# Kernel optimization log

Hardware: AMD Instinct MI355X
Metric: run time of the kernel (lower is better)

Reference implementation:

```python
import jax, jax.numpy as jnp
import numpy as np


def _to_complex(t):
    # last dim 2 = (real, imag) -> complex64
    return jax.lax.complex(t[..., 0], t[..., 1])


def setup_inputs() -> dict:
    key = jax.random.key(0)
    k1, k2, k3, k4 = jax.random.split(key, 4)
    N, C_out, C_in, H, Wf = 2, 64, 3, 256, 129  # Wf = 256//2 + 1 (rfft width)
    X = jax.random.normal(k1, (N, 1, C_in, H, Wf, 2), dtype=jnp.float32)
    D = jax.random.normal(k2, (N, C_out, C_in, H, Wf, 2), dtype=jnp.float32)
    Y = jax.random.normal(k3, (N, C_out, 1, H, Wf, 2), dtype=jnp.float32)
    # alpha is a positive penalty weight; offset away from 0 to avoid blow-up in Z/alpha
    alpha = jax.random.uniform(k4, (N, 1, 1, 1), dtype=jnp.float32) + 0.5
    x_size = np.array([256, 256], dtype=np.int64)  # spatial size for irfft2
    return {"X": X, "D": D, "Y": Y, "alpha": alpha, "x_size": x_size}


def reference(X, D, Y, alpha, x_size):
    C_in = X.shape[2]
    Xc = _to_complex(X)  # (N,1,C_in,H,Wf)
    Dc = _to_complex(D)  # (N,C_out,C_in,H,Wf)
    Yc = _to_complex(Y)  # (N,C_out,1,H,Wf)
    # alpha.unsqueeze(-1).unsqueeze(-1)/C_in: in complex repr one extra axis suffices
    a = (alpha / C_in)[..., None]  # (N,1,1,1,1), real, broadcasts over (N,C_out,C_in,H,Wf)
    Dconj = jnp.conj(Dc)
    Z = Yc * Dc + a * Xc  # (N,C_out,C_in,H,Wf)
    factor1 = Z / a
    numerator = jnp.sum(Dconj * Z, axis=2, keepdims=True)  # (N,C_out,1,H,Wf)
    # csum adds a real scalar (alpha^2) to the real part only
    denominator = a * jnp.sum(Dconj * Dc, axis=2, keepdims=True) + a ** 2
    factor2 = Dc * (numerator / denominator)  # (N,C_out,C_in,H,Wf)
    Xhat = jnp.mean(factor1 - factor2, axis=1)  # (N,C_in,H,Wf)
    Hs, Ws = int(x_size[0]), int(x_size[1])
    # torch.irfft(signal_ndim=2, normalized=False) == full (1/n-normalized) inverse rfft2
    return jnp.fft.irfftn(Xhat, s=(Hs, Ws), axes=(-2, -1))
```

## Files before the change

kernel.cpp:

```cpp
#include <hip/hip_runtime.h>
#include <math.h>

#define H_   256
#define Wf_  129
#define HWf_ 33024
#define CIN_ 3
#define COUT_ 64
#define TW_  0.0245436926f

typedef float f32x4 __attribute__((ext_vector_type(4)));

__global__ __launch_bounds__(256) void solve_stage1(
    const float* __restrict__ X, const float* __restrict__ D,
    const float* __restrict__ Y, const float* __restrict__ alpha,
    float* __restrict__ Xhat)
{
    const int tid  = threadIdx.x;
    const int pl   = tid & 15;
    const int cog  = tid >> 4;
    const int pair = blockIdx.x * 16 + pl;
    const int pos0 = pair * 2;
    const int n    = pos0 / HWf_;
    const int hw0  = pos0 - n * HWf_;

    const float a    = alpha[n] * (1.0f / 3.0f);
    const float inva = 1.0f / a;
    const float a2   = a * a;

    f32x4 x[3];
#pragma unroll
    for (int ci = 0; ci < 3; ++ci)
        x[ci] = *(const f32x4*)(X + ((size_t)(n * 3 + ci) * HWf_ + hw0) * 2);

    const int co0 = cog * 4;
    const float* Dp = D + ((size_t)(n * 64 + co0) * 3) * (HWf_ * 2) + hw0 * 2;
    const float* Yp = Y + ((size_t)(n * 64 + co0)) * (HWf_ * 2) + hw0 * 2;

    float acc[12];
#pragma unroll
    for (int q = 0; q < 12; ++q) acc[q] = 0.f;

#pragma unroll
    for (int co = 0; co < 4; ++co) {
        f32x4 y  = __builtin_nontemporal_load(
                       (const f32x4*)(Yp + (size_t)co * (HWf_ * 2)));
        f32x4 d0 = __builtin_nontemporal_load(
                       (const f32x4*)(Dp + (size_t)(co * 3 + 0) * (HWf_ * 2)));
        f32x4 d1 = __builtin_nontemporal_load(
                       (const f32x4*)(Dp + (size_t)(co * 3 + 1) * (HWf_ * 2)));
        f32x4 d2 = __builtin_nontemporal_load(
                       (const f32x4*)(Dp + (size_t)(co * 3 + 2) * (HWf_ * 2)));

        {
            float s2 = d0[0]*d0[0] + d0[1]*d0[1] + d1[0]*d1[0] + d1[1]*d1[1]
                     + d2[0]*d2[0] + d2[1]*d2[1];
            float sr = d0[0]*x[0][0] + d0[1]*x[0][1] + d1[0]*x[1][0] + d1[1]*x[1][1]
                     + d2[0]*x[2][0] + d2[1]*x[2][1];
            float si = d0[0]*x[0][1] - d0[1]*x[0][0] + d1[0]*x[1][1] - d1[1]*x[1][0]
                     + d2[0]*x[2][1] - d2[1]*x[2][0];
            float nr = y[0] * s2 + a * sr, ni = y[1] * s2 + a * si;
            float invden = 1.0f / (a * s2 + a2);
            float tr = y[0] * inva - nr * invden;
            float ti = y[1] * inva - ni * invden;
            acc[0] += d0[0]*tr - d0[1]*ti;  acc[1] += d0[0]*ti + d0[1]*tr;
            acc[2] += d1[0]*tr - d1[1]*ti;  acc[3] += d1[0]*ti + d1[1]*tr;
            acc[4] += d2[0]*tr - d2[1]*ti;  acc[5] += d2[0]*ti + d2[1]*tr;
        }
        {
            float s2 = d0[2]*d0[2] + d0[3]*d0[3] + d1[2]*d1[2] + d1[3]*d1[3]
                     + d2[2]*d2[2] + d2[3]*d2[3];
            float sr = d0[2]*x[0][2] + d0[3]*x[0][3] + d1[2]*x[1][2] + d1[3]*x[1][3]
                     + d2[2]*x[2][2] + d2[3]*x[2][3];
            float si = d0[2]*x[0][3] - d0[3]*x[0][2] + d1[2]*x[1][3] - d1[3]*x[1][2]
                     + d2[2]*x[2][3] - d2[3]*x[2][2];
            float nr = y[2] * s2 + a * sr, ni = y[3] * s2 + a * si;
            float invden = 1.0f / (a * s2 + a2);
            float tr = y[2] * inva - nr * invden;
            float ti = y[3] * inva - ni * invden;
            acc[6]  += d0[2]*tr - d0[3]*ti;  acc[7]  += d0[2]*ti + d0[3]*tr;
            acc[8]  += d1[2]*tr - d1[3]*ti;  acc[9]  += d1[2]*ti + d1[3]*tr;
            acc[10] += d2[2]*tr - d2[3]*ti;  acc[11] += d2[2]*ti + d2[3]*tr;
        }
    }

    __shared__ float red[16 * 192];
    {
        const int base = cog * 192 + pl * 12;
#pragma unroll
        for (int q = 0; q < 12; ++q) red[base + q] = acc[q];
    }
    __syncthreads();

    if (tid < 192) {
        float s = 0.f;
#pragma unroll
        for (int c = 0; c < 16; ++c) s += red[c * 192 + tid];
        const int P   = tid / 12;
        const int r   = tid - P * 12;
        const int pos = r / 6;
        const int rr  = r - pos * 6;
        const int ci  = rr >> 1;
        const int cc  = rr & 1;
        const int gp  = (blockIdx.x * 16 + P) * 2 + pos;
        const int hw  = gp - n * HWf_;
        const size_t o = ((size_t)(n * 3 + ci) * HWf_ + hw) * 2 + cc;
        Xhat[o] = X[o] + s * (1.0f / 64.0f);
    }
}

__global__ __launch_bounds__(128) void solve_stage2(
    const float2* __restrict__ in, float2* __restrict__ out)
{
    __shared__ float2 col[256];

    const int b    = blockIdx.x;
    const int n_ci = b / Wf_;
    const int w    = b - n_ci * Wf_;
    const int t    = threadIdx.x;

    const float2* src = in + (size_t)n_ci * HWf_ + w;
    col[t]       = src[t * Wf_];
    col[t + 128] = src[(t + 128) * Wf_];
    __syncthreads();

    float wc, wsn;
    sincosf((float)t * TW_, &wsn, &wc);

    float ar = 0.f, ai = 0.f, br = 0.f, bi = 0.f;
    for (int kb = 0; kb < 8; ++kb) {
        const int k0 = kb * 32;
        float tr, ti;
        {
            const int m = (t * k0) & 255;
            float s, c; sincosf((float)m * TW_, &s, &c);
            tr = c; ti = s;
        }
#pragma unroll
        for (int j = 0; j < 32; ++j) {
            const float2 v = col[k0 + j];
            const float pr = v.x * tr - v.y * ti;
            const float pi = v.x * ti + v.y * tr;
            ar += pr; ai += pi;
            if ((k0 + j) & 1) { br -= pr; bi -= pi; }
            else             { br += pr; bi += pi; }
            const float nt = tr * wc - ti * wsn;
            ti = tr * wsn + ti * wc;
            tr = nt;
        }
    }

    float2* dst = out + (size_t)n_ci * HWf_ + w;
    dst[t * Wf_]         = make_float2(ar * (1.0f / 256.0f), ai * (1.0f / 256.0f));
    dst[(t + 128) * Wf_] = make_float2(br * (1.0f / 256.0f), bi * (1.0f / 256.0f));
}

__global__ __launch_bounds__(128) void solve_stage3(
    const float2* __restrict__ in, float* __restrict__ out)
{
    __shared__ float2 row[Wf_];

    const int b = blockIdx.x;
    const int t = threadIdx.x;

    row[t] = in[(size_t)b * Wf_ + t];
    if (t == 0) row[128] = in[(size_t)b * Wf_ + 128];
    __syncthreads();

    float wc, wsn;
    sincosf((float)t * TW_, &wsn, &wc);

    float sa = 0.f, sb = 0.f;
    for (int kb = 0; kb < 4; ++kb) {
        const int k0 = kb * 32;
        float tr, ti;
        {
            const int m = (t * k0) & 255;
            float s, c; sincosf((float)m * TW_, &s, &c);
            tr = c; ti = s;
        }
#pragma unroll
        for (int j = 0; j < 32; ++j) {
            const float2 v = row[k0 + j];
            const float pr = v.x * tr - v.y * ti;
            sa += pr;
            if ((k0 + j) & 1) sb -= pr; else sb += pr;
            const float nt = tr * wc - ti * wsn;
            ti = tr * wsn + ti * wc;
            tr = nt;
        }
    }

    const float sgn  = (t & 1) ? -1.0f : 1.0f;
    const float base = -0.5f * row[0].x + sgn * 0.5f * row[128].x;
    out[(size_t)b * 256 + t]       = (sa + base) * (1.0f / 128.0f);
    out[(size_t)b * 256 + t + 128] = (sb + base) * (1.0f / 128.0f);
}

extern "C" void kernel_launch(void* const* d_in, const int* in_sizes, int n_in,
                              void* d_out, int out_size, void* d_ws, size_t ws_size,
                              hipStream_t stream) {
    const float* X     = (const float*)d_in[0];
    const float* D     = (const float*)d_in[1];
    const float* Y     = (const float*)d_in[2];
    const float* alpha = (const float*)d_in[3];

    float* ws1 = (float*)d_ws;
    float2* ws2 = (float2*)(ws1 + (size_t)CIN_ * 2 * HWf_ * 2);

    solve_stage1<<<2064, 256, 0, stream>>>(X, D, Y, alpha, ws1);
    solve_stage2<<<2 * CIN_ * Wf_, 128, 0, stream>>>((const float2*)ws1, ws2);
    solve_stage3<<<2 * CIN_ * H_, 128, 0, stream>>>(ws2, (float*)d_out);
}
```

Measured before the change: 204.4 us.

## Store intermediate spectrum column-major so column FFT reads contiguously

Stage 1 now writes Xhat transposed to (n,ci,w,h), so the column inverse DFT in stage 2 reads and writes contiguous 256-element columns instead of reads strided by Wf. Stage 2 packs two columns per 256-thread block. Stage 3 now does the strided gather from the transposed layout when loading each row, and writes its output with nontemporal stores. The aim is cheaper memory access in the DFT stages, at the cost of scattered writes in stage 1 and strided reads in stage 3.

```diff
diff --git a/kernel.cpp b/kernel.cpp
--- a/kernel.cpp
+++ b/kernel.cpp
@@ -103,24 +103,26 @@
         const int cc  = rr & 1;
         const int gp  = (blockIdx.x * 16 + P) * 2 + pos;
         const int hw  = gp - n * HWf_;
-        const size_t o = ((size_t)(n * 3 + ci) * HWf_ + hw) * 2 + cc;
-        Xhat[o] = X[o] + s * (1.0f / 64.0f);
-    }
-}
-
-__global__ __launch_bounds__(128) void solve_stage2(
+        const int h   = hw / Wf_;
+        const int w   = hw - h * Wf_;
+        const size_t so = ((size_t)(n * 3 + ci) * HWf_ + hw) * 2 + cc;
+        const size_t o = (((size_t)(n * 3 + ci) * Wf_ + w) * H_ + h) * 2 + cc;
+        Xhat[o] = X[so] + s * (1.0f / 64.0f);
+    }
+}
+
+__global__ __launch_bounds__(256) void solve_stage2(
     const float2* __restrict__ in, float2* __restrict__ out)
 {
-    __shared__ float2 col[256];
-
-    const int b    = blockIdx.x;
-    const int n_ci = b / Wf_;
-    const int w    = b - n_ci * Wf_;
-    const int t    = threadIdx.x;
-
-    const float2* src = in + (size_t)n_ci * HWf_ + w;
-    col[t]       = src[t * Wf_];
-    col[t + 128] = src[(t + 128) * Wf_];
+    __shared__ float2 col[2][256];
+
+    const int b   = blockIdx.x;
+    const int sub = threadIdx.x >> 7;
+    const int t   = threadIdx.x & 127;
+
+    const float2* src = in + ((size_t)b * 2 + sub) * H_;
+    col[sub][t]       = src[t];
+    col[sub][t + 128] = src[t + 128];
     __syncthreads();
 
     float wc, wsn;
@@ -137,7 +139,7 @@
         }
 #pragma unroll
         for (int j = 0; j < 32; ++j) {
-            const float2 v = col[k0 + j];
+            const float2 v = col[sub][k0 + j];
             const float pr = v.x * tr - v.y * ti;
             const float pi = v.x * ti + v.y * tr;
             ar += pr; ai += pi;
@@ -149,9 +151,9 @@
         }
     }
 
-    float2* dst = out + (size_t)n_ci * HWf_ + w;
-    dst[t * Wf_]         = make_float2(ar * (1.0f / 256.0f), ai * (1.0f / 256.0f));
-    dst[(t + 128) * Wf_] = make_float2(br * (1.0f / 256.0f), bi * (1.0f / 256.0f));
+    float2* dst = out + ((size_t)b * 2 + sub) * H_;
+    dst[t]       = make_float2(ar * (1.0f / 256.0f), ai * (1.0f / 256.0f));
+    dst[t + 128] = make_float2(br * (1.0f / 256.0f), bi * (1.0f / 256.0f));
 }
 
 __global__ __launch_bounds__(128) void solve_stage3(
@@ -159,11 +161,13 @@
 {
     __shared__ float2 row[Wf_];
 
-    const int b = blockIdx.x;
-    const int t = threadIdx.x;
-
-    row[t] = in[(size_t)b * Wf_ + t];
-    if (t == 0) row[128] = in[(size_t)b * Wf_ + 128];
+    const int b    = blockIdx.x;
+    const int n_ci = b >> 8;
+    const int h    = b & 255;
+    const int t    = threadIdx.x;
+
+    row[t] = in[((size_t)n_ci * Wf_ + t) * H_ + h];
+    if (t == 0) row[128] = in[((size_t)n_ci * Wf_ + 128) * H_ + h];
     __syncthreads();
 
     float wc, wsn;
@@ -192,8 +196,10 @@
 
     const float sgn  = (t & 1) ? -1.0f : 1.0f;
     const float base = -0.5f * row[0].x + sgn * 0.5f * row[128].x;
-    out[(size_t)b * 256 + t]       = (sa + base) * (1.0f / 128.0f);
-    out[(size_t)b * 256 + t + 128] = (sb + base) * (1.0f / 128.0f);
+    __builtin_nontemporal_store((sa + base) * (1.0f / 128.0f),
+                                out + (size_t)b * 256 + t);
+    __builtin_nontemporal_store((sb + base) * (1.0f / 128.0f),
+                                out + (size_t)b * 256 + t + 128);
 }
 
 extern "C" void kernel_launch(void* const* d_in, const int* in_sizes, int n_in,
@@ -208,6 +214,6 @@
     float2* ws2 = (float2*)(ws1 + (size_t)CIN_ * 2 * HWf_ * 2);
 
     solve_stage1<<<2064, 256, 0, stream>>>(X, D, Y, alpha, ws1);
-    solve_stage2<<<2 * CIN_ * Wf_, 128, 0, stream>>>((const float2*)ws1, ws2);
+    solve_stage2<<<(2 * CIN_ * Wf_) / 2, 256, 0, stream>>>((const float2*)ws1, ws2);
     solve_stage3<<<2 * CIN_ * H_, 128, 0, stream>>>(ws2, (float*)d_out);
 }
```

New measurement: 200.2 us. 1.02x faster.
